# Optimization experiments

Hardware: AMD Instinct MI355X
Metric: run time of the kernel (lower is better)

## Reference

```python
import jax, jax.numpy as jnp
import numpy as np

B, T, DIM, H = 2, 2048, 1024, 16
DH = DIM // H  # head dim = 64, rope half = 32


def _apply_rope(q, k):
    # q,k: [b,h,t,d]
    b, h, t, d = q.shape
    half = d // 2
    idx = jnp.arange(half, dtype=jnp.float32)
    pos = jnp.arange(t, dtype=jnp.float32)[:, None]
    inv = 10000.0 ** (-2.0 * idx / (2.0 * half))
    ang = pos * inv  # [t, half]
    cos = jnp.cos(ang).astype(q.dtype)[None, None]  # [1,1,t,half]
    sin = jnp.sin(ang).astype(q.dtype)[None, None]

    def rot(x):
        a = x[..., :half]
        b2 = x[..., half:2 * half]
        return jnp.concatenate([a * cos - b2 * sin, a * sin + b2 * cos], axis=-1)

    return rot(q), rot(k)


def setup_inputs() -> dict:
    key = jax.random.key(0)
    k0, k1, k2 = jax.random.split(key, 3)
    x = jax.random.normal(k0, (B, T, DIM), dtype=jnp.float32)
    mask = jnp.tril(jnp.ones((T, T), dtype=jnp.int32))[None, None]  # causal [1,1,T,T]
    scale = DIM ** -0.5
    W_qkv = jax.random.normal(k1, (DIM, 3 * DIM), dtype=jnp.float32) * scale
    b_qkv = jnp.zeros((3 * DIM,), dtype=jnp.float32)
    W_out = jax.random.normal(k2, (DIM, DIM), dtype=jnp.float32) * scale
    b_out = jnp.zeros((DIM,), dtype=jnp.float32)
    return {"x": x, "mask": mask, "W_qkv": W_qkv, "b_qkv": b_qkv,
            "W_out": W_out, "b_out": b_out}


def reference(x, mask, W_qkv, b_qkv, W_out, b_out):
    b, t, c = x.shape
    qkv = x @ W_qkv + b_qkv  # [b,t,3c]
    q, k, v = jnp.split(qkv, 3, axis=-1)
    q = q.reshape(b, t, H, DH).transpose(0, 2, 1, 3)  # [b,h,t,dh]
    k = k.reshape(b, t, H, DH).transpose(0, 2, 1, 3)
    v = v.reshape(b, t, H, DH).transpose(0, 2, 1, 3)
    q, k = _apply_rope(q, k)
    s = jnp.einsum('bhqd,bhkd->bhqk', q, k) * (DH ** -0.5)
    s = jnp.where(mask == 0, -jnp.inf, s)
    p = jax.nn.softmax(s, axis=-1)  # dropout is identity (drop=0.0)
    y = jnp.einsum('bhqk,bhkd->bhqd', p, v)
    y = y.transpose(0, 2, 1, 3).reshape(b, t, c)
    return y @ W_out + b_out
```

## Files before the change

kernel.cpp:

```cpp
#include <hip/hip_runtime.h>
#include <hip/hip_bf16.h>
#include <math.h>
#include <type_traits>

#define BB 2
#define TT 2048
#define DIMM 1024
#define HH 16
#define DHH 64

typedef _Float16 half8_t __attribute__((ext_vector_type(8)));
typedef _Float16 half4_t __attribute__((ext_vector_type(4)));
typedef float floatx4 __attribute__((ext_vector_type(4)));

typedef const unsigned int __attribute__((address_space(1)))* gp_t;
typedef unsigned int __attribute__((address_space(3)))* lp_t;

__device__ __forceinline__ void async16(const void* g, void* l) {
    __builtin_amdgcn_global_load_lds((gp_t)g, (lp_t)l, 16, 0, 0);
}

template <int N>
__device__ __forceinline__ void vwait() {
    asm volatile("s_waitcnt vmcnt(%0)" :: "n"(N) : "memory");
}

__global__ __launch_bounds__(256) void prep_kernel(
    const float* __restrict__ x, _Float16* __restrict__ xb,
    const float* __restrict__ W_qkv, _Float16* __restrict__ Wqt,
    const float* __restrict__ W_out, _Float16* __restrict__ Wot,
    float2* __restrict__ tab) {
    __shared__ float tile[32][33];
    int bid = blockIdx.x, tid = threadIdx.x;
    if (bid < 4096) {
        int i = (bid * 256 + tid) * 4;
        floatx4 v = *(const floatx4*)(x + i);
        half4_t h;
        h[0] = (_Float16)v[0]; h[1] = (_Float16)v[1];
        h[2] = (_Float16)v[2]; h[3] = (_Float16)v[3];
        *(half4_t*)(xb + i) = h;
    } else if (bid < 8192) {
        const float* W; _Float16* Wt; int K, N, bx, by;
        if (bid < 7168) {
            W = W_qkv; Wt = Wqt; K = 1024; N = 3072;
            int b2 = bid - 4096; bx = b2 % 96; by = b2 / 96;
        } else {
            W = W_out; Wt = Wot; K = 1024; N = 1024;
            int b2 = bid - 7168; bx = b2 & 31; by = b2 >> 5;
        }
        int n0 = bx * 32, k0 = by * 32;
        int tx = tid & 31, ty = tid >> 5;
        for (int i = 0; i < 32; i += 8)
            tile[ty + i][tx] = W[(size_t)(k0 + ty + i) * N + n0 + tx];
        __syncthreads();
        for (int i = 0; i < 32; i += 8)
            Wt[(size_t)(n0 + ty + i) * K + k0 + tx] = (_Float16)tile[tx][ty + i];
    } else {
        int idx = (bid - 8192) * 256 + tid;
        int t = idx >> 5, d = idx & 31;
        float inv = __expf(-(float)d * 0.28782313662425572f);
        float ang = (float)t * inv;
        float s, c;
        __sincosf(ang, &s, &c);
        tab[idx] = make_float2(c, s);
    }
}

template <int BN, int MODE>
__global__ __launch_bounds__(256) void gemm_ld_kernel(
    const _Float16* __restrict__ A, const _Float16* __restrict__ Bt,
    const float* __restrict__ bias, float* __restrict__ C,
    _Float16* __restrict__ Qr, _Float16* __restrict__ Kr, _Float16* __restrict__ Vt,
    const float2* __restrict__ tab,
    int M, int N, int K) {
    constexpr int NB = (BN == 128) ? 4 : 2;
    constexpr int BCH = BN * 32;
    constexpr int BOFF = 3 * 4096;
    __shared__ __align__(16) _Float16 smem[3 * 4096 + 3 * BCH];
    int tid = threadIdx.x;
    int m0 = blockIdx.y * 128, n0 = blockIdx.x * BN;
    int wave = tid >> 6, lane = tid & 63;
    int wm = (wave & 1) * 64;
    int wn = (wave >> 1) * (BN / 2);
    int lm = lane & 15, quad = lane >> 4;

    floatx4 acc[4][NB] = {};

    int arow = tid >> 2, ach = tid & 3;
    int acol = ((ach ^ (arow & 3)) << 3);

    auto stage = [&](int k0, int buf) {
        _Float16* Ab = smem + buf * 4096;
        _Float16* Bb = smem + BOFF + buf * BCH;
        async16(A + (size_t)(m0 + arow) * K + k0 + acol, (char*)Ab + tid * 16);
        async16(A + (size_t)(m0 + 64 + arow) * K + k0 + acol, (char*)Ab + (256 + tid) * 16);
        async16(Bt + (size_t)(n0 + arow) * K + k0 + acol, (char*)Bb + tid * 16);
        if (BN == 128)
            async16(Bt + (size_t)(n0 + 64 + arow) * K + k0 + acol, (char*)Bb + (256 + tid) * 16);
    };

    int nIt = K >> 5;
    stage(0, 0);
    stage(32, 1);
    int fsw = (quad ^ (lm & 3)) << 3;
    for (int it = 0; it < nIt; ++it) {
        int buf = it % 3;
        if (it < nIt - 1) {
            if (BN == 128) asm volatile("s_waitcnt vmcnt(4)" ::: "memory");
            else           asm volatile("s_waitcnt vmcnt(3)" ::: "memory");
        } else {
            asm volatile("s_waitcnt vmcnt(0)" ::: "memory");
        }
        asm volatile("s_barrier" ::: "memory");
        if (it + 2 < nIt) stage((it + 2) << 5, (it + 2) % 3);

        const _Float16* Ab = smem + buf * 4096;
        const _Float16* Bb = smem + BOFF + buf * BCH;
        half8_t af[4], bf[NB];
        for (int mb = 0; mb < 4; mb++)
            af[mb] = *(const half8_t*)&Ab[(wm + mb * 16 + lm) * 32 + fsw];
        for (int nb = 0; nb < NB; nb++)
            bf[nb] = *(const half8_t*)&Bb[(wn + nb * 16 + lm) * 32 + fsw];
        for (int mb = 0; mb < 4; mb++)
            for (int nb = 0; nb < NB; nb++)
                acc[mb][nb] = __builtin_amdgcn_mfma_f32_16x16x32_f16(af[mb], bf[nb], acc[mb][nb], 0, 0, 0);
    }

    if (MODE == 0) {
        for (int mb = 0; mb < 4; mb++) {
            int row = m0 + wm + mb * 16 + quad * 4;
            for (int nb = 0; nb < NB; nb++) {
                int col = n0 + wn + nb * 16 + lm;
                float bv = bias[col];
                for (int r = 0; r < 4; r++)
                    C[(size_t)(row + r) * N + col] = acc[mb][nb][r] + bv;
            }
        }
    }
}

__global__ __launch_bounds__(512, 2) void qkv_gemm256(
    const _Float16* __restrict__ A, const _Float16* __restrict__ Bt,
    const float* __restrict__ bias,
    _Float16* __restrict__ Qr, _Float16* __restrict__ Kr, _Float16* __restrict__ Vt,
    const float2* __restrict__ tab) {
    constexpr int K = 1024;
    __shared__ __align__(16) _Float16 smem[65536];
    int tid = threadIdx.x;
    int m0 = blockIdx.y * 256, n0 = blockIdx.x * 256;
    int wave = tid >> 6, lane = tid & 63;
    int wm = (wave & 1) * 128;
    int wn = (wave >> 1) * 64;
    int lm = lane & 15, quad = lane >> 4;

    int srow = tid >> 3;
    int sch8 = ((tid & 7) ^ (srow & 7)) << 3;

    auto stageA = [&](int kt, int buf, int half) {
        const _Float16* s = A + (size_t)(m0 + srow + half * 64) * K + kt * 64 + sch8;
        char* d = (char*)smem + buf * 32768 + half * 8192 + tid * 16;
        async16(s, d);
        async16(s + (size_t)128 * K, d + 16384);
    };
    auto stageB = [&](int kt, int buf, int half) {
#pragma unroll
        for (int i = 0; i < 2; i++) {
            int rowbase = (i * 2 + (wave >> 2)) * 64 + half * 32 + (wave & 3) * 8;
            int row = rowbase + (lane >> 3);
            const _Float16* s = Bt + (size_t)(n0 + row) * K + kt * 64 +
                                (((lane & 7) ^ (row & 7)) << 3);
            char* d = (char*)smem + 65536 + buf * 32768 + rowbase * 128 + lane * 16;
            async16(s, d);
        }
    };

    int ch0 = (quad ^ (lm & 7)) << 3;
    int ch1 = ((4 + quad) ^ (lm & 7)) << 3;

    floatx4 acc[8][4] = {};
    half8_t af[4][2], bf[4][2];

    stageA(0, 0, 0);
    stageB(0, 0, 0);
    stageB(0, 0, 1);
    stageA(0, 0, 1);

    auto tileStep = [&](auto lastc, int kt) {
        constexpr bool LAST = decltype(lastc)::value;
        int cb = kt & 1, nb = cb ^ 1;
        const _Float16* Ap = smem + cb * 16384 + (wm + lm) * 64;
        const _Float16* Bp = smem + 32768 + cb * 16384 + (wn + lm) * 64;

        vwait<4>();
        __builtin_amdgcn_s_barrier();
#pragma unroll
        for (int mf = 0; mf < 4; mf++) {
            af[mf][0] = *(const half8_t*)(Ap + mf * 1024 + ch0);
            af[mf][1] = *(const half8_t*)(Ap + mf * 1024 + ch1);
        }
#pragma unroll
        for (int nf = 0; nf < 2; nf++) {
            bf[nf][0] = *(const half8_t*)(Bp + nf * 1024 + ch0);
            bf[nf][1] = *(const half8_t*)(Bp + nf * 1024 + ch1);
        }
        if constexpr (!LAST) stageA(kt + 1, nb, 0);
        __builtin_amdgcn_s_setprio(1);
#pragma unroll
        for (int mf = 0; mf < 4; mf++)
#pragma unroll
            for (int nf = 0; nf < 2; nf++) {
                acc[mf][nf] = __builtin_amdgcn_mfma_f32_16x16x32_f16(af[mf][0], bf[nf][0], acc[mf][nf], 0, 0, 0);
                acc[mf][nf] = __builtin_amdgcn_mfma_f32_16x16x32_f16(af[mf][1], bf[nf][1], acc[mf][nf], 0, 0, 0);
            }
        __builtin_amdgcn_s_setprio(0);

        vwait<LAST ? 2 : 4>();
        __builtin_amdgcn_s_barrier();
#pragma unroll
        for (int nf = 2; nf < 4; nf++) {
            bf[nf][0] = *(const half8_t*)(Bp + nf * 1024 + ch0);
            bf[nf][1] = *(const half8_t*)(Bp + nf * 1024 + ch1);
        }
        if constexpr (!LAST) stageB(kt + 1, nb, 0);
        __builtin_amdgcn_s_setprio(1);
#pragma unroll
        for (int mf = 0; mf < 4; mf++)
#pragma unroll
            for (int nf = 2; nf < 4; nf++) {
                acc[mf][nf] = __builtin_amdgcn_mfma_f32_16x16x32_f16(af[mf][0], bf[nf][0], acc[mf][nf], 0, 0, 0);
                acc[mf][nf] = __builtin_amdgcn_mfma_f32_16x16x32_f16(af[mf][1], bf[nf][1], acc[mf][nf], 0, 0, 0);
            }
        __builtin_amdgcn_s_setprio(0);

        vwait<LAST ? 0 : 4>();
        __builtin_amdgcn_s_barrier();
#pragma unroll
        for (int mf = 0; mf < 4; mf++) {
            af[mf][0] = *(const half8_t*)(Ap + (4 + mf) * 1024 + ch0);
            af[mf][1] = *(const half8_t*)(Ap + (4 + mf) * 1024 + ch1);
        }
        if constexpr (!LAST) stageB(kt + 1, nb, 1);
        __builtin_amdgcn_s_setprio(1);
#pragma unroll
        for (int mf = 0; mf < 4; mf++)
#pragma unroll
            for (int nf = 2; nf < 4; nf++) {
                acc[4 + mf][nf] = __builtin_amdgcn_mfma_f32_16x16x32_f16(af[mf][0], bf[nf][0], acc[4 + mf][nf], 0, 0, 0);
                acc[4 + mf][nf] = __builtin_amdgcn_mfma_f32_16x16x32_f16(af[mf][1], bf[nf][1], acc[4 + mf][nf], 0, 0, 0);
            }
        __builtin_amdgcn_s_setprio(0);

        __builtin_amdgcn_s_barrier();
        if constexpr (!LAST) stageA(kt + 1, nb, 1);
        __builtin_amdgcn_s_setprio(1);
#pragma unroll
        for (int mf = 0; mf < 4; mf++)
#pragma unroll
            for (int nf = 0; nf < 2; nf++) {
                acc[4 + mf][nf] = __builtin_amdgcn_mfma_f32_16x16x32_f16(af[mf][0], bf[nf][0], acc[4 + mf][nf], 0, 0, 0);
                acc[4 + mf][nf] = __builtin_amdgcn_mfma_f32_16x16x32_f16(af[mf][1], bf[nf][1], acc[4 + mf][nf], 0, 0, 0);
            }
        __builtin_amdgcn_s_setprio(0);
    };

    for (int kt = 0; kt < 15; ++kt)
        tileStep(std::integral_constant<bool, false>{}, kt);
    tileStep(std::integral_constant<bool, true>{}, 15);

    __syncthreads();
    _Float16* scratch = smem + wave * 8192;
    int col0 = n0 + wn;
    int sect = col0 >> 10;
    int h = (col0 & 1023) >> 6;
    int b = (m0 + wm) >> 11;
    int tbase = (m0 + wm) & 2047;
    if (sect < 2) {
        _Float16* dst = (sect == 0) ? Qr : Kr;
        float fscale = (sect == 0) ? 0.18033688011112042f : 1.0f;
#pragma unroll
        for (int nb = 0; nb < 2; nb++) {
            int d = nb * 16 + lm;
            float bva = bias[col0 + d];
            float bvb = bias[col0 + d + 32];
            int d2 = d + 32;
#pragma unroll
            for (int mf = 0; mf < 8; mf++) {
#pragma unroll
                for (int r = 0; r < 4; r++) {
                    int tl = mf * 16 + quad * 4 + r;
                    float2 cs = tab[(tbase + tl) * 32 + d];
                    float va = acc[mf][nb][r] + bva;
                    float vb = acc[mf][nb + 2][r] + bvb;
                    int sw = tl & 7;
                    scratch[tl * 64 + (((d >> 3) ^ sw) << 3) + (d & 7)] =
                        (_Float16)((va * cs.x - vb * cs.y) * fscale);
                    scratch[tl * 64 + (((d2 >> 3) ^ sw) << 3) + (d2 & 7)] =
                        (_Float16)((va * cs.y + vb * cs.x) * fscale);
                }
            }
        }
        asm volatile("s_waitcnt lgkmcnt(0)" ::: "memory");
        size_t ob = (size_t)(b * HH + h) * TT + tbase;
        for (int j = 0; j < 16; j++) {
            int row = j * 8 + (lane >> 3);
            int c2 = lane & 7;
            half8_t v = *(const half8_t*)&scratch[row * 64 + ((c2 ^ (row & 7)) << 3)];
            *(half8_t*)&dst[(ob + row) * 64 + c2 * 8] = v;
        }
    } else {
#pragma unroll
        for (int nf = 0; nf < 4; nf++) {
            int d = nf * 16 + lm;
            float bv = bias[col0 + d];
            int sw = d & 7;
#pragma unroll
            for (int mf = 0; mf < 8; mf++) {
                int t0 = mf * 16 + quad * 4;
                int tc = t0 >> 3;
                half4_t pv;
#pragma unroll
                for (int r = 0; r < 4; r++) pv[r] = (_Float16)(acc[mf][nf][r] + bv);
                *(half4_t*)&scratch[d * 128 + (((tc & 8) | ((tc & 7) ^ sw)) << 3) + (t0 & 7)] = pv;
            }
        }
        asm volatile("s_waitcnt lgkmcnt(0)" ::: "memory");
        size_t vb0 = (size_t)(b * HH + h) * 64;
        for (int j = 0; j < 16; j++) {
            int drow = j * 4 + (lane >> 4);
            int c2 = lane & 15;
            int ptc = (c2 & 8) | ((c2 & 7) ^ (drow & 7));
            half8_t v = *(const half8_t*)&scratch[drow * 128 + (ptc << 3)];
            *(half8_t*)&Vt[(vb0 + drow) * TT + tbase + c2 * 8] = v;
        }
    }
}

__device__ const unsigned char kBlkMap[24] = {
    30, 26, 22, 20, 18, 16, 14, 31,
    28, 24, 12, 29, 10, 27, 8, 25,
    0, 17, 2, 19, 4, 21, 6, 23};

__global__ __launch_bounds__(256, 3) void flash_attn(
    const _Float16* __restrict__ Qr, const _Float16* __restrict__ Kr,
    const _Float16* __restrict__ Vt,
    _Float16* __restrict__ Po, float* __restrict__ Pls, _Float16* __restrict__ Yb) {
    int bh = blockIdx.y;
    int code = kBlkMap[blockIdx.x];
    int iq = code >> 1, ic = code & 1;
    int kstart = ic * 16;
    int kend = min(kstart + 16, 2 * iq + 2);
    bool full = (ic == 0) && (kend == 2 * iq + 2);

    int tid = threadIdx.x, wave = tid >> 6, lane = tid & 63;
    int lm = lane & 15, quad = lane >> 4;
    int q0w = iq * 128 + wave * 32;

    __shared__ __align__(16) _Float16 Ks[2][64 * 64];
    __shared__ __align__(16) _Float16 Vs[2][64 * 64];
    __shared__ __align__(16) _Float16 Pbuf[4][32 * 64];
    _Float16* plds = Pbuf[wave];

    const _Float16* Qbase = Qr + ((size_t)bh * TT + q0w) * 64;
    half8_t aq[2][2];
    for (int mb = 0; mb < 2; mb++) {
        aq[mb][0] = *(const half8_t*)(Qbase + (size_t)(mb * 16 + lm) * 64 + quad * 8);
        aq[mb][1] = *(const half8_t*)(Qbase + (size_t)(mb * 16 + lm) * 64 + 32 + quad * 8);
    }

    const _Float16* Kb = Kr + (size_t)bh * TT * 64;
    const _Float16* Vb = Vt + (size_t)bh * 64 * TT;

    floatx4 o[2][4] = {};
    float lsum[2] = {};

    auto stage = [&](int kt, int buf) {
        int k0 = kt * 64;
        for (int i = 0; i < 2; i++) {
            int sl = i * 256 + tid;
            int row = sl >> 3;
            int c = (sl & 7) ^ (row & 7);
            async16(Kb + (size_t)(k0 + row) * 64 + c * 8, (char*)&Ks[buf][0] + sl * 16);
            async16(Vb + (size_t)row * TT + k0 + c * 8, (char*)&Vs[buf][0] + sl * 16);
        }
    };

    stage(kstart, 0);

    for (int kt = kstart; kt < kend; ++kt) {
        int buf = (kt - kstart) & 1;
        __syncthreads();
        if (kt + 1 < kend) stage(kt + 1, buf ^ 1);
        int k0 = kt * 64;
        if (k0 > q0w + 31) continue;

        floatx4 s4[4][2] = {};
        __builtin_amdgcn_s_setprio(1);
        for (int kb = 0; kb < 4; kb++) {
            int row = kb * 16 + lm, sw = row & 7;
            half8_t kf0 = *(const half8_t*)&Ks[buf][row * 64 + ((quad ^ sw) << 3)];
            half8_t kf1 = *(const half8_t*)&Ks[buf][row * 64 + (((4 + quad) ^ sw) << 3)];
            for (int qb = 0; qb < 2; qb++) {
                s4[kb][qb] = __builtin_amdgcn_mfma_f32_16x16x32_f16(kf0, aq[qb][0], s4[kb][qb], 0, 0, 0);
                s4[kb][qb] = __builtin_amdgcn_mfma_f32_16x16x32_f16(kf1, aq[qb][1], s4[kb][qb], 0, 0, 0);
            }
        }
        __builtin_amdgcn_s_setprio(0);

        if (k0 + 63 > q0w) {
            for (int kb = 0; kb < 4; kb++)
                for (int qb = 0; qb < 2; qb++) {
                    int krow = k0 + kb * 16 + quad * 4;
                    int qcol = q0w + qb * 16 + lm;
                    for (int r = 0; r < 4; r++)
                        if (krow + r > qcol) s4[kb][qb][r] = -1e30f;
                }
        }

        for (int qb = 0; qb < 2; qb++) {
            int q = qb * 16 + lm;
            int swz = q & 7;
            for (int kb = 0; kb < 4; kb++) {
                float p0 = __builtin_amdgcn_exp2f(s4[kb][qb][0]);
                float p1 = __builtin_amdgcn_exp2f(s4[kb][qb][1]);
                float p2 = __builtin_amdgcn_exp2f(s4[kb][qb][2]);
                float p3 = __builtin_amdgcn_exp2f(s4[kb][qb][3]);
                lsum[qb] += (p0 + p1) + (p2 + p3);
                half4_t pk;
                pk[0] = (_Float16)p0; pk[1] = (_Float16)p1;
                pk[2] = (_Float16)p2; pk[3] = (_Float16)p3;
                int c = kb * 2 + (quad >> 1);
                *(half4_t*)&plds[q * 64 + ((c ^ swz) << 3) + (quad & 1) * 4] = pk;
            }
        }
        asm volatile("s_waitcnt lgkmcnt(0)" ::: "memory");
        int psw = lm & 7;
        half8_t pa[2][2];
        for (int mp = 0; mp < 2; mp++) {
            pa[mp][0] = *(const half8_t*)&plds[(mp * 16 + lm) * 64 + ((quad ^ psw) << 3)];
            pa[mp][1] = *(const half8_t*)&plds[(mp * 16 + lm) * 64 + (((4 + quad) ^ psw) << 3)];
        }
        asm volatile("" ::: "memory");

        __builtin_amdgcn_s_setprio(1);
        for (int db = 0; db < 4; db++) {
            int row = db * 16 + lm, sw = row & 7;
            half8_t vb0 = *(const half8_t*)&Vs[buf][row * 64 + ((quad ^ sw) << 3)];
            half8_t vb1 = *(const half8_t*)&Vs[buf][row * 64 + (((4 + quad) ^ sw) << 3)];
            for (int mb = 0; mb < 2; mb++) {
                o[mb][db] = __builtin_amdgcn_mfma_f32_16x16x32_f16(pa[mb][0], vb0, o[mb][db], 0, 0, 0);
                o[mb][db] = __builtin_amdgcn_mfma_f32_16x16x32_f16(pa[mb][1], vb1, o[mb][db], 0, 0, 0);
            }
        }
        __builtin_amdgcn_s_setprio(0);
    }

    float ltot[2];
    for (int qb = 0; qb < 2; qb++) {
        float v = lsum[qb];
        v += __shfl_xor(v, 16);
        v += __shfl_xor(v, 32);
        ltot[qb] = v;
    }
    float lred[2][4];
    for (int mb = 0; mb < 2; mb++)
        for (int r = 0; r < 4; r++)
            lred[mb][r] = __shfl(ltot[mb], quad * 4 + r);

    for (int mb = 0; mb < 2; mb++)
        for (int db = 0; db < 4; db++) {
            int cbase = db * 2 + (lm >> 3);
            for (int r = 0; r < 4; r++) {
                int prow = mb * 16 + quad * 4 + r;
                float v = o[mb][db][r];
                if (full) v /= lred[mb][r];
                plds[prow * 64 + ((cbase ^ (prow & 7)) << 3) + (lm & 7)] = (_Float16)v;
            }
        }
    asm volatile("s_waitcnt lgkmcnt(0)" ::: "memory");
    int b = bh >> 4, h = bh & 15;
    size_t pbase = ((size_t)(bh * 16 + iq) * 2 + ic) * 8192;
    for (int j = 0; j < 4; j++) {
        int row = j * 8 + (lane >> 3);
        int c = lane & 7;
        half8_t v = *(const half8_t*)&plds[row * 64 + ((c ^ (row & 7)) << 3)];
        if (full) {
            size_t yb = ((size_t)(b * TT) + iq * 128 + wave * 32 + row) * DIMM + h * 64 + c * 8;
            *(half8_t*)&Yb[yb] = v;
        } else {
            *(half8_t*)&Po[pbase + (wave * 32 + row) * 64 + c * 8] = v;
        }
    }
    if (!full && lm == 0) {
        size_t lb = ((size_t)(bh * 16 + iq) * 2 + ic) * 128;
        for (int mb = 0; mb < 2; mb++)
            for (int r = 0; r < 4; r++)
                Pls[lb + wave * 32 + mb * 16 + quad * 4 + r] = lred[mb][r];
    }
}

__global__ __launch_bounds__(256) void attn_combine(
    const _Float16* __restrict__ Po, const float* __restrict__ Pls,
    _Float16* __restrict__ Yb) {
    int iq = blockIdx.x + 8, bh = blockIdx.y;
    int b = bh >> 4, h = bh & 15;
    int tid = threadIdx.x;
    int row = tid >> 1, cg = (tid & 1) * 32;

    size_t base = ((size_t)(bh * 16 + iq) * 2) * 8192 + row * 64 + cg;
    size_t lb = ((size_t)(bh * 16 + iq) * 2) * 128 + row;
    float l = Pls[lb] + Pls[lb + 128];
    float inv = 1.0f / l;
    const half8_t* p0 = (const half8_t*)&Po[base];
    const half8_t* p1 = (const half8_t*)&Po[base + 8192];
    size_t yb = ((size_t)(b * TT) + iq * 128 + row) * DIMM + h * 64 + cg;
    for (int j = 0; j < 4; j++) {
        half8_t a = p0[j], c = p1[j], v;
        for (int i = 0; i < 8; i++)
            v[i] = (_Float16)(((float)a[i] + (float)c[i]) * inv);
        *(half8_t*)&Yb[yb + j * 8] = v;
    }
}

extern "C" void kernel_launch(void* const* d_in, const int* in_sizes, int n_in,
                              void* d_out, int out_size, void* d_ws, size_t ws_size,
                              hipStream_t stream) {
    const float* x = (const float*)d_in[0];
    const float* W_qkv = (const float*)d_in[2];
    const float* b_qkv = (const float*)d_in[3];
    const float* W_out = (const float*)d_in[4];
    const float* b_out = (const float*)d_in[5];
    float* out = (float*)d_out;

    char* ws = (char*)d_ws;
    _Float16* xb = (_Float16*)ws;   ws += (size_t)4096 * 1024 * 2;
    _Float16* Wqt = (_Float16*)ws;  ws += (size_t)3072 * 1024 * 2;
    _Float16* Wot = (_Float16*)ws;  ws += (size_t)1024 * 1024 * 2;
    _Float16* Qr = (_Float16*)ws;   ws += (size_t)32 * 2048 * 64 * 2;
    _Float16* Kr = (_Float16*)ws;   ws += (size_t)32 * 2048 * 64 * 2;
    _Float16* Vt = (_Float16*)ws;   ws += (size_t)32 * 2048 * 64 * 2;
    _Float16* Yb = (_Float16*)ws;   ws += (size_t)4096 * 1024 * 2;
    float2* tab = (float2*)ws;      ws += (size_t)2048 * 32 * 8;
    _Float16* Po = (_Float16*)ws;   ws += (size_t)32 * 16 * 2 * 8192 * 2;
    float* Pls = (float*)ws;        ws += (size_t)32 * 16 * 2 * 128 * 4;

    prep_kernel<<<8448, 256, 0, stream>>>(x, xb, W_qkv, Wqt, W_out, Wot, tab);

    qkv_gemm256<<<dim3(12, 16), 512, 0, stream>>>(
        xb, Wqt, b_qkv, Qr, Kr, Vt, tab);

    flash_attn<<<dim3(24, 32), 256, 0, stream>>>(Qr, Kr, Vt, Po, Pls, Yb);
    attn_combine<<<dim3(8, 32), 256, 0, stream>>>(Po, Pls, Yb);

    gemm_ld_kernel<128, 0><<<dim3(8, 32), 256, 0, stream>>>(
        Yb, Wot, b_out, out, nullptr, nullptr, nullptr, nullptr, 4096, 1024, 1024);
}
```

Measured before the change: 181.7 us.

## Load B operand directly from global into registers, bypassing LDS

The QKV projection GEMM no longer stages the B (weight) tile through LDS. Each wave now loads its own B fragments straight from global memory into double-buffered registers one k-tile ahead, which cuts the per-tile phases from four to two and removes two barriers per tile. The goal is less LDS traffic and fewer synchronisation points. In exchange, B is no longer shared across waves through LDS, so global and L2 traffic per block rises, register pressure goes up, and the vmcnt wait counts are retuned to match.

```diff
diff --git a/kernel.cpp b/kernel.cpp
--- a/kernel.cpp
+++ b/kernel.cpp
@@ -162,110 +162,77 @@
         async16(s, d);
         async16(s + (size_t)128 * K, d + 16384);
     };
-    auto stageB = [&](int kt, int buf, int half) {
-#pragma unroll
-        for (int i = 0; i < 2; i++) {
-            int rowbase = (i * 2 + (wave >> 2)) * 64 + half * 32 + (wave & 3) * 8;
-            int row = rowbase + (lane >> 3);
-            const _Float16* s = Bt + (size_t)(n0 + row) * K + kt * 64 +
-                                (((lane & 7) ^ (row & 7)) << 3);
-            char* d = (char*)smem + 65536 + buf * 32768 + rowbase * 128 + lane * 16;
-            async16(s, d);
-        }
+
+    const _Float16* Bbase = Bt + (size_t)(n0 + wn + lm) * K + quad * 8;
+    auto loadB = [&](int kt, half8_t (*bf)[2]) {
+#pragma unroll
+        for (int nf = 0; nf < 4; nf++)
+#pragma unroll
+            for (int kh = 0; kh < 2; kh++)
+                bf[nf][kh] = *(const half8_t*)(Bbase + (size_t)nf * 16 * K + kt * 64 + kh * 32);
     };
 
     int ch0 = (quad ^ (lm & 7)) << 3;
     int ch1 = ((4 + quad) ^ (lm & 7)) << 3;
 
     floatx4 acc[8][4] = {};
-    half8_t af[4][2], bf[4][2];
+    half8_t af[4][2];
+    half8_t bA[4][2], bB[4][2];
 
     stageA(0, 0, 0);
-    stageB(0, 0, 0);
-    stageB(0, 0, 1);
+    loadB(0, bA);
     stageA(0, 0, 1);
 
-    auto tileStep = [&](auto lastc, int kt) {
+    auto tileStep = [&](auto lastc, int kt, half8_t (*bcur)[2], half8_t (*bnext)[2]) {
         constexpr bool LAST = decltype(lastc)::value;
-        int cb = kt & 1, nb = cb ^ 1;
+        int cb = kt & 1, nb2 = cb ^ 1;
         const _Float16* Ap = smem + cb * 16384 + (wm + lm) * 64;
-        const _Float16* Bp = smem + 32768 + cb * 16384 + (wn + lm) * 64;
-
-        vwait<4>();
+
+        vwait<10>();
         __builtin_amdgcn_s_barrier();
 #pragma unroll
         for (int mf = 0; mf < 4; mf++) {
             af[mf][0] = *(const half8_t*)(Ap + mf * 1024 + ch0);
             af[mf][1] = *(const half8_t*)(Ap + mf * 1024 + ch1);
         }
-#pragma unroll
-        for (int nf = 0; nf < 2; nf++) {
-            bf[nf][0] = *(const half8_t*)(Bp + nf * 1024 + ch0);
-            bf[nf][1] = *(const half8_t*)(Bp + nf * 1024 + ch1);
-        }
-        if constexpr (!LAST) stageA(kt + 1, nb, 0);
+        if constexpr (!LAST) { stageA(kt + 1, nb2, 0); loadB(kt + 1, bnext); }
         __builtin_amdgcn_s_setprio(1);
 #pragma unroll
         for (int mf = 0; mf < 4; mf++)
 #pragma unroll
-            for (int nf = 0; nf < 2; nf++) {
-                acc[mf][nf] = __builtin_amdgcn_mfma_f32_16x16x32_f16(af[mf][0], bf[nf][0], acc[mf][nf], 0, 0, 0);
-                acc[mf][nf] = __builtin_amdgcn_mfma_f32_16x16x32_f16(af[mf][1], bf[nf][1], acc[mf][nf], 0, 0, 0);
+            for (int nf = 0; nf < 4; nf++) {
+                acc[mf][nf] = __builtin_amdgcn_mfma_f32_16x16x32_f16(af[mf][0], bcur[nf][0], acc[mf][nf], 0, 0, 0);
+                acc[mf][nf] = __builtin_amdgcn_mfma_f32_16x16x32_f16(af[mf][1], bcur[nf][1], acc[mf][nf], 0, 0, 0);
             }
         __builtin_amdgcn_s_setprio(0);
 
-        vwait<LAST ? 2 : 4>();
-        __builtin_amdgcn_s_barrier();
-#pragma unroll
-        for (int nf = 2; nf < 4; nf++) {
-            bf[nf][0] = *(const half8_t*)(Bp + nf * 1024 + ch0);
-            bf[nf][1] = *(const half8_t*)(Bp + nf * 1024 + ch1);
-        }
-        if constexpr (!LAST) stageB(kt + 1, nb, 0);
-        __builtin_amdgcn_s_setprio(1);
-#pragma unroll
-        for (int mf = 0; mf < 4; mf++)
-#pragma unroll
-            for (int nf = 2; nf < 4; nf++) {
-                acc[mf][nf] = __builtin_amdgcn_mfma_f32_16x16x32_f16(af[mf][0], bf[nf][0], acc[mf][nf], 0, 0, 0);
-                acc[mf][nf] = __builtin_amdgcn_mfma_f32_16x16x32_f16(af[mf][1], bf[nf][1], acc[mf][nf], 0, 0, 0);
-            }
-        __builtin_amdgcn_s_setprio(0);
-
-        vwait<LAST ? 0 : 4>();
+        vwait<LAST ? 0 : 10>();
         __builtin_amdgcn_s_barrier();
 #pragma unroll
         for (int mf = 0; mf < 4; mf++) {
             af[mf][0] = *(const half8_t*)(Ap + (4 + mf) * 1024 + ch0);
             af[mf][1] = *(const half8_t*)(Ap + (4 + mf) * 1024 + ch1);
         }
-        if constexpr (!LAST) stageB(kt + 1, nb, 1);
+        if constexpr (!LAST) stageA(kt + 1, nb2, 1);
         __builtin_amdgcn_s_setprio(1);
 #pragma unroll
         for (int mf = 0; mf < 4; mf++)
 #pragma unroll
-            for (int nf = 2; nf < 4; nf++) {
-                acc[4 + mf][nf] = __builtin_amdgcn_mfma_f32_16x16x32_f16(af[mf][0], bf[nf][0], acc[4 + mf][nf], 0, 0, 0);
-                acc[4 + mf][nf] = __builtin_amdgcn_mfma_f32_16x16x32_f16(af[mf][1], bf[nf][1], acc[4 + mf][nf], 0, 0, 0);
-            }
-        __builtin_amdgcn_s_setprio(0);
-
-        __builtin_amdgcn_s_barrier();
-        if constexpr (!LAST) stageA(kt + 1, nb, 1);
-        __builtin_amdgcn_s_setprio(1);
-#pragma unroll
-        for (int mf = 0; mf < 4; mf++)
-#pragma unroll
-            for (int nf = 0; nf < 2; nf++) {
-                acc[4 + mf][nf] = __builtin_amdgcn_mfma_f32_16x16x32_f16(af[mf][0], bf[nf][0], acc[4 + mf][nf], 0, 0, 0);
-                acc[4 + mf][nf] = __builtin_amdgcn_mfma_f32_16x16x32_f16(af[mf][1], bf[nf][1], acc[4 + mf][nf], 0, 0, 0);
+            for (int nf = 0; nf < 4; nf++) {
+                acc[4 + mf][nf] = __builtin_amdgcn_mfma_f32_16x16x32_f16(af[mf][0], bcur[nf][0], acc[4 + mf][nf], 0, 0, 0);
+                acc[4 + mf][nf] = __builtin_amdgcn_mfma_f32_16x16x32_f16(af[mf][1], bcur[nf][1], acc[4 + mf][nf], 0, 0, 0);
             }
         __builtin_amdgcn_s_setprio(0);
     };
 
-    for (int kt = 0; kt < 15; ++kt)
-        tileStep(std::integral_constant<bool, false>{}, kt);
-    tileStep(std::integral_constant<bool, true>{}, 15);
+    constexpr auto F = std::integral_constant<bool, false>{};
+    constexpr auto L = std::integral_constant<bool, true>{};
+    for (int kt = 0; kt < 14; kt += 2) {
+        tileStep(F, kt, bA, bB);
+        tileStep(F, kt + 1, bB, bA);
+    }
+    tileStep(F, 14, bA, bB);
+    tileStep(L, 15, bB, bA);
 
     __syncthreads();
     _Float16* scratch = smem + wave * 8192;
```

Result: slower. 202.1 us (+11.3%).
